# Kernel tuning notes

Hardware: AMD Instinct MI355X
Metric: run time of the kernel (lower is better)

The kernel has to match this reference:

```python
import jax, jax.numpy as jnp
import numpy as np

# --- SOM geometry constants (match init_kwargs) ---
MAP_ROWS, MAP_COLS = 32, 32
N_PROTO = MAP_ROWS * MAP_COLS
SIGMA = 1.0
PBC = True


def _build_neighborhood():
    """Gaussian neighborhood h[i,j]=exp(-dist(i,j)^2/(2*sigma^2)) on a hexagonal
    grid with periodic boundary conditions (faithful to Neighborhoods(...,'Hexagons','grid',PBC=True))."""
    rr, cc = np.meshgrid(np.arange(MAP_ROWS), np.arange(MAP_COLS), indexing='ij')
    # hexagonal lattice coordinates: odd rows shifted by 0.5, row spacing sqrt(3)/2
    x = cc + 0.5 * (rr % 2)
    y = rr * (np.sqrt(3.0) / 2.0)
    pos = np.stack([x.ravel(), y.ravel()], axis=1).astype(np.float64)  # [M, 2]
    diff = pos[:, None, :] - pos[None, :, :]                            # [M, M, 2]
    if PBC:
        width = float(MAP_COLS)
        height = MAP_ROWS * (np.sqrt(3.0) / 2.0)
        d2 = np.full((N_PROTO, N_PROTO), np.inf)
        for sx in (-1.0, 0.0, 1.0):
            for sy in (-1.0, 0.0, 1.0):
                dx = diff[..., 0] + sx * width
                dy = diff[..., 1] + sy * height
                d2 = np.minimum(d2, dx * dx + dy * dy)
    else:
        d2 = (diff ** 2).sum(-1)
    return np.exp(-d2 / (2.0 * SIGMA ** 2)).astype(np.float32)         # [M, M]


H = jnp.asarray(_build_neighborhood())  # constant [M, M] neighborhood matrix


def setup_inputs() -> dict:
    key = jax.random.key(0)
    k1, k2 = jax.random.split(key)
    inputs = jax.random.normal(k1, (16384, 256), dtype=jnp.float32)
    prototypes = jax.random.normal(k2, (N_PROTO, 256), dtype=jnp.float32) * 0.05
    return {"inputs": inputs, "prototypes": prototypes}


def reference(inputs, prototypes):
    # squared euclidean distances d[n, m] = ||x_n - p_m||^2, computed without
    # materializing the (N, M, D) broadcast intermediate
    x2 = jnp.sum(inputs * inputs, axis=1, keepdims=True)        # [N, 1]
    p2 = jnp.sum(prototypes * prototypes, axis=1)               # [M]
    d = x2 - 2.0 * (inputs @ prototypes.T) + p2[None, :]        # [N, M]
    energies = H @ d.T                                          # [M, N]
    bmus = jnp.argmin(energies, axis=0)                         # [N]
    out = 0.5 * jnp.take_along_axis(energies, bmus[None, :], axis=0)  # [1, N]
    return out
```

## Files before the change

### kernel.cpp

```cpp
#include <hip/hip_runtime.h>
#include <hip/hip_bf16.h>
#include <math.h>

#define D 256
#define NPROTO 1024
#define WR 13
#define WC 18
#define WJ (WR * WC)
#define JSUB 59
#define GMAT_BLOCKS (NPROTO / 4)
#define XPREP_BLOCKS (16384 / 8)

#define WAITVM(N) asm volatile("s_waitcnt vmcnt(" #N ")" ::: "memory")

typedef __attribute__((ext_vector_type(8))) short short8;
typedef __attribute__((ext_vector_type(4))) float f32x4;

__device__ __forceinline__ short f2bf(float f) {
    union { __hip_bfloat16 b; short s; } u;
    u.b = __float2bfloat16(f);
    return u.s;
}

__device__ __forceinline__ void gload_lds16(void* lds, const void* g) {
    __builtin_amdgcn_global_load_lds(
        (const __attribute__((address_space(1))) unsigned*)g,
        (__attribute__((address_space(3))) unsigned*)lds, 16, 0, 0);
}

__device__ __forceinline__ void proto_pos(int idx, double& x, double& y) {
    int r = idx >> 5, c = idx & 31;
    x = (double)c + 0.5 * (double)(r & 1);
    y = (double)r * 0.86602540378443864676;
}

__device__ __forceinline__ float hval(int i, int j) {
    double xi, yi, xj, yj;
    proto_pos(i, xi, yi);
    proto_pos(j, xj, yj);
    double dx0 = xi - xj, dy0 = yi - yj;
    const double W = 32.0;
    const double Hh = 27.712812921102035;
    double best = 1e300;
#pragma unroll
    for (int sx = -1; sx <= 1; ++sx) {
        double dx = dx0 + (double)sx * W;
#pragma unroll
        for (int sy = -1; sy <= 1; ++sy) {
            double dy = dy0 + (double)sy * Hh;
            double d2 = dx * dx + dy * dy;
            best = fmin(best, d2);
        }
    }
    return (float)exp(-0.5 * best);
}

__global__ void __launch_bounds__(256) prep_kernel(
    const float* __restrict__ X, const float* __restrict__ P,
    short* __restrict__ Xg, short* __restrict__ GbF,
    float* __restrict__ x2, float* __restrict__ hsum, float* __restrict__ hp2,
    unsigned* __restrict__ out) {
    int t = threadIdx.x;
    int bx = blockIdx.x;

    if (bx >= GMAT_BLOCKS) {
        int row = (bx - GMAT_BLOCKS) * 8 + (t >> 5);
        int g = t & 31;
        const float4* src = reinterpret_cast<const float4*>(X + (size_t)row * D) + g * 2;
        float4 a = src[0], b = src[1];
        float s = a.x * a.x + a.y * a.y + a.z * a.z + a.w * a.w +
                  b.x * b.x + b.y * b.y + b.z * b.z + b.w * b.w;
        s += __shfl_xor(s, 1);
        s += __shfl_xor(s, 2);
        s += __shfl_xor(s, 4);
        s += __shfl_xor(s, 8);
        s += __shfl_xor(s, 16);
        if (g == 0) x2[row] = s;
        short8 w;
        w[0] = f2bf(a.x); w[1] = f2bf(a.y); w[2] = f2bf(a.z); w[3] = f2bf(a.w);
        w[4] = f2bf(b.x); w[5] = f2bf(b.y); w[6] = f2bf(b.z); w[7] = f2bf(b.w);
        int sw = ((g * 8) & 63) ^ ((row & 7) << 3);
        *reinterpret_cast<short8*>(Xg + (size_t)row * D + ((g >> 3) << 6) + sw) = w;
        if (t < 8) out[(bx - GMAT_BLOCKS) * 8 + t] = 0x7f800000u;
        return;
    }

    __shared__ float ht[4][WJ];
    __shared__ int jrow[WJ];
    __shared__ __align__(16) float gpart[4][4][256];
    __shared__ float hqred[4][4];
    __shared__ float hsred[4][4];
    int i0 = bx * 4;
    int r0 = i0 >> 5, c0 = i0 & 31;

    for (int u = t; u < WJ; u += 256) {
        int jr = (r0 + (u / WC) - 6 + 32) & 31;
        int jc = (c0 + (u % WC) - 7 + 32) & 31;
        int j = jr * 32 + jc;
        jrow[u] = j;
#pragma unroll
        for (int s = 0; s < 4; ++s) ht[s][u] = hval(i0 + s, j);
    }
    __syncthreads();

    int w = t >> 6, lane = t & 63;
    int j0 = w * JSUB;
    int j1 = (j0 + JSUB < WJ) ? j0 + JSUB : WJ;
    f32x4 g[4] = {{0.f, 0.f, 0.f, 0.f}, {0.f, 0.f, 0.f, 0.f},
                  {0.f, 0.f, 0.f, 0.f}, {0.f, 0.f, 0.f, 0.f}};
    float hqp[4] = {0.f, 0.f, 0.f, 0.f};
    float hsp[4] = {0.f, 0.f, 0.f, 0.f};
    for (int u = j0; u < j1; ++u) {
        f32x4 pv = *reinterpret_cast<const f32x4*>(P + (size_t)jrow[u] * D + lane * 4);
        float q = pv[0] * pv[0] + pv[1] * pv[1] + pv[2] * pv[2] + pv[3] * pv[3];
#pragma unroll
        for (int s = 0; s < 4; ++s) {
            float h = ht[s][u];
            g[s][0] = fmaf(h, pv[0], g[s][0]);
            g[s][1] = fmaf(h, pv[1], g[s][1]);
            g[s][2] = fmaf(h, pv[2], g[s][2]);
            g[s][3] = fmaf(h, pv[3], g[s][3]);
            hqp[s] = fmaf(h, q, hqp[s]);
            hsp[s] += h;
        }
    }
#pragma unroll
    for (int s = 0; s < 4; ++s)
        *reinterpret_cast<f32x4*>(&gpart[w][s][lane * 4]) = g[s];
#pragma unroll
    for (int s = 0; s < 4; ++s) {
#pragma unroll
        for (int off = 1; off < 64; off <<= 1) hqp[s] += __shfl_xor(hqp[s], off);
    }
    if (lane == 0) {
#pragma unroll
        for (int s = 0; s < 4; ++s) { hqred[w][s] = hqp[s]; hsred[w][s] = hsp[s]; }
    }
    __syncthreads();

    {
        int s = t >> 6;
        f32x4 gs = *reinterpret_cast<const f32x4*>(&gpart[0][s][lane * 4]);
#pragma unroll
        for (int ww = 1; ww < 4; ++ww) {
            f32x4 gp = *reinterpret_cast<const f32x4*>(&gpart[ww][s][lane * 4]);
            gs[0] += gp[0]; gs[1] += gp[1]; gs[2] += gp[2]; gs[3] += gp[3];
        }
        float h0 = __shfl_down(gs[0], 1);
        float h1 = __shfl_down(gs[1], 1);
        float h2 = __shfl_down(gs[2], 1);
        float h3 = __shfl_down(gs[3], 1);
        if (!(lane & 1)) {
            int c = lane >> 1;
            int kg = c >> 2;
            int q = c & 3;
            int i = i0 + s;
            int Ig = i >> 4;
            short8 wv;
            wv[0] = f2bf(gs[0]); wv[1] = f2bf(gs[1]); wv[2] = f2bf(gs[2]); wv[3] = f2bf(gs[3]);
            wv[4] = f2bf(h0);    wv[5] = f2bf(h1);    wv[6] = f2bf(h2);    wv[7] = f2bf(h3);
            *reinterpret_cast<short8*>(
                GbF + ((size_t)(Ig * 8 + kg) << 9) + ((i & 15) + 16 * q) * 8) = wv;
        }
    }
    if (t < 4) {
        hsum[i0 + t] = hsred[0][t] + hsred[1][t] + hsred[2][t] + hsred[3][t];
    } else if (t < 8) {
        int s = t - 4;
        hp2[i0 + s] = hqred[0][s] + hqred[1][s] + hqred[2][s] + hqred[3][s];
    }
}

__global__ void __launch_bounds__(256) som7_kernel(
    const short* __restrict__ Xg, const short* __restrict__ GbF,
    const float* __restrict__ x2, const float* __restrict__ hsum,
    const float* __restrict__ hp2, unsigned* __restrict__ out) {
    __shared__ __align__(16) short Xs[2][128 * 64];
    __shared__ float red[2][128];

    const int t = threadIdx.x;
    const int lane = t & 63;
    const int wid = t >> 6;
    const int wr = wid >> 1;
    const int wc = wid & 1;
    const int lm = lane & 15;
    const int lq = lane >> 4;
    const int n0 = blockIdx.x * 128;
    const int ib0 = blockIdx.y * 128;
    const int Igbase = (ib0 >> 4) + wc * 4;

    f32x4 acc[4][4];
#pragma unroll
    for (int m = 0; m < 4; ++m)
#pragma unroll
        for (int n = 0; n < 4; ++n) acc[m][n] = (f32x4){0.f, 0.f, 0.f, 0.f};

    auto stage_X = [&](int xb, int kt) {
#pragma unroll
        for (int q = 0; q < 4; ++q) {
            int row = q * 32 + (t >> 3);
            gload_lds16((char*)(&Xs[xb][0]) + q * 4096 + t * 16,
                        Xg + (size_t)(n0 + row) * D + kt * 64 + (t & 7) * 8);
        }
    };

    stage_X(0, 0);

#pragma unroll
    for (int kt = 0; kt < 4; ++kt) {
        short8 b0[4], b1[4];
#pragma unroll
        for (int n = 0; n < 4; ++n) {
            const short* fb = GbF + ((size_t)((Igbase + n) * 8 + kt * 2) << 9) + lane * 8;
            b0[n] = *reinterpret_cast<const short8*>(fb);
            b1[n] = *reinterpret_cast<const short8*>(fb + 512);
        }
        __builtin_amdgcn_sched_barrier(0);
        if (kt < 3) stage_X((kt + 1) & 1, kt + 1);
        if (kt < 3) { WAITVM(12); } else { WAITVM(8); }
        __builtin_amdgcn_sched_barrier(0);
        __builtin_amdgcn_s_barrier();

        const short* xb = &Xs[kt & 1][0];
        {
            const int off = (lq * 8) ^ ((lm & 7) << 3);
            short8 a[4];
#pragma unroll
            for (int m = 0; m < 4; ++m)
                a[m] = *reinterpret_cast<const short8*>(
                    &xb[(wr * 64 + m * 16 + lm) * 64 + off]);
            if (kt < 3) { WAITVM(8); } else { WAITVM(4); }
            __builtin_amdgcn_s_setprio(1);
#pragma unroll
            for (int m = 0; m < 4; ++m)
#pragma unroll
                for (int n = 0; n < 4; ++n)
                    acc[m][n] = __builtin_amdgcn_mfma_f32_16x16x32_bf16(a[m], b0[n], acc[m][n], 0, 0, 0);
            __builtin_amdgcn_s_setprio(0);
        }
        {
            const int off = (32 + lq * 8) ^ ((lm & 7) << 3);
            short8 a[4];
#pragma unroll
            for (int m = 0; m < 4; ++m)
                a[m] = *reinterpret_cast<const short8*>(
                    &xb[(wr * 64 + m * 16 + lm) * 64 + off]);
            if (kt < 3) { WAITVM(4); } else { WAITVM(0); }
            __builtin_amdgcn_s_setprio(1);
#pragma unroll
            for (int m = 0; m < 4; ++m)
#pragma unroll
                for (int n = 0; n < 4; ++n)
                    acc[m][n] = __builtin_amdgcn_mfma_f32_16x16x32_bf16(a[m], b1[n], acc[m][n], 0, 0, 0);
            __builtin_amdgcn_s_setprio(0);
        }
    }

    float x2v[4][4];
#pragma unroll
    for (int m = 0; m < 4; ++m)
#pragma unroll
        for (int j = 0; j < 4; ++j)
            x2v[m][j] = x2[n0 + wr * 64 + m * 16 + lq * 4 + j];

    float rmin[4][4];
#pragma unroll
    for (int m = 0; m < 4; ++m)
#pragma unroll
        for (int j = 0; j < 4; ++j) rmin[m][j] = 3.4e38f;

#pragma unroll
    for (int ni = 0; ni < 4; ++ni) {
        int ig = ib0 + wc * 64 + ni * 16 + lm;
        float hs = hsum[ig];
        float hq = hp2[ig];
#pragma unroll
        for (int m = 0; m < 4; ++m)
#pragma unroll
            for (int j = 0; j < 4; ++j) {
                float e = fmaf(hs, x2v[m][j], hq) - 2.0f * acc[m][ni][j];
                rmin[m][j] = fminf(rmin[m][j], e);
            }
    }

#pragma unroll
    for (int m = 0; m < 4; ++m)
#pragma unroll
        for (int j = 0; j < 4; ++j) {
            float v = rmin[m][j];
            v = fminf(v, __shfl_xor(v, 1));
            v = fminf(v, __shfl_xor(v, 2));
            v = fminf(v, __shfl_xor(v, 4));
            v = fminf(v, __shfl_xor(v, 8));
            rmin[m][j] = v;
        }
    if (lm == 0) {
#pragma unroll
        for (int m = 0; m < 4; ++m)
#pragma unroll
            for (int j = 0; j < 4; ++j)
                red[wc][wr * 64 + m * 16 + lq * 4 + j] = rmin[m][j];
    }
    __syncthreads();
    if (t < 128) {
        float v = fminf(red[0][t], red[1][t]);
        atomicMin(out + n0 + t, __float_as_uint(0.5f * v));
    }
}

extern "C" void kernel_launch(void* const* d_in, const int* in_sizes, int n_in,
                              void* d_out, int out_size, void* d_ws, size_t ws_size,
                              hipStream_t stream) {
    const float* X = (const float*)d_in[0];
    const float* P = (const float*)d_in[1];
    unsigned* out = (unsigned*)d_out;
    int N = in_sizes[0] / D;

    float* ws = (float*)d_ws;
    float* hsum = ws + 1024;
    float* hp2 = ws + 2048;
    float* x2 = ws + 4096;
    short* GbF = (short*)(ws + 32768);
    short* Xg = (short*)(ws + 262144);

    prep_kernel<<<GMAT_BLOCKS + XPREP_BLOCKS, 256, 0, stream>>>(
        X, P, Xg, GbF, x2, hsum, hp2, out);
    som7_kernel<<<dim3(N / 128, NPROTO / 128), 256, 0, stream>>>(
        Xg, GbF, x2, hsum, hp2, out);
}
```

Baseline: 34.58 us.

## Keep input tile in registers and sweep all prototypes per block

The X preprocessing now writes inputs in MFMA fragment order through an LDS transpose, so the main kernel can load its A operands straight into registers instead of staging them via LDS. The main kernel covers all 1024 prototypes per 64-row block, with 8 waves each sweeping a quarter of the prototypes. It reduces the minimum across waves in LDS and writes the output directly. This removes the atomicMin, the output initialisation and the LDS double-buffer pipeline. The trade-off is that every block streams the whole G matrix from cache, and the grid is a single dimension of 256 blocks, which may lower parallelism and raise register pressure.

```diff
diff --git a/kernel.cpp b/kernel.cpp
--- a/kernel.cpp
+++ b/kernel.cpp
@@ -8,10 +8,8 @@
 #define WC 18
 #define WJ (WR * WC)
 #define JSUB 59
-#define GMAT_BLOCKS (NPROTO / 4)
-#define XPREP_BLOCKS (16384 / 8)
-
-#define WAITVM(N) asm volatile("s_waitcnt vmcnt(" #N ")" ::: "memory")
+#define GMAT_BLOCKS 256
+#define XPREP_BLOCKS 512
 
 typedef __attribute__((ext_vector_type(8))) short short8;
 typedef __attribute__((ext_vector_type(4))) float f32x4;
@@ -20,12 +18,6 @@
     union { __hip_bfloat16 b; short s; } u;
     u.b = __float2bfloat16(f);
     return u.s;
-}
-
-__device__ __forceinline__ void gload_lds16(void* lds, const void* g) {
-    __builtin_amdgcn_global_load_lds(
-        (const __attribute__((address_space(1))) unsigned*)g,
-        (__attribute__((address_space(3))) unsigned*)lds, 16, 0, 0);
 }
 
 __device__ __forceinline__ void proto_pos(int idx, double& x, double& y) {
@@ -55,33 +47,49 @@
     return (float)exp(-0.5 * best);
 }
 
+
 __global__ void __launch_bounds__(256) prep_kernel(
     const float* __restrict__ X, const float* __restrict__ P,
-    short* __restrict__ Xg, short* __restrict__ GbF,
-    float* __restrict__ x2, float* __restrict__ hsum, float* __restrict__ hp2,
-    unsigned* __restrict__ out) {
+    short* __restrict__ XgF, short* __restrict__ GbF,
+    float* __restrict__ x2, float* __restrict__ hsum, float* __restrict__ hp2) {
     int t = threadIdx.x;
     int bx = blockIdx.x;
 
     if (bx >= GMAT_BLOCKS) {
-        int row = (bx - GMAT_BLOCKS) * 8 + (t >> 5);
-        int g = t & 31;
-        const float4* src = reinterpret_cast<const float4*>(X + (size_t)row * D) + g * 2;
-        float4 a = src[0], b = src[1];
-        float s = a.x * a.x + a.y * a.y + a.z * a.z + a.w * a.w +
-                  b.x * b.x + b.y * b.y + b.z * b.z + b.w * b.w;
-        s += __shfl_xor(s, 1);
-        s += __shfl_xor(s, 2);
-        s += __shfl_xor(s, 4);
-        s += __shfl_xor(s, 8);
-        s += __shfl_xor(s, 16);
-        if (g == 0) x2[row] = s;
-        short8 w;
-        w[0] = f2bf(a.x); w[1] = f2bf(a.y); w[2] = f2bf(a.z); w[3] = f2bf(a.w);
-        w[4] = f2bf(b.x); w[5] = f2bf(b.y); w[6] = f2bf(b.z); w[7] = f2bf(b.w);
-        int sw = ((g * 8) & 63) ^ ((row & 7) << 3);
-        *reinterpret_cast<short8*>(Xg + (size_t)row * D + ((g >> 3) << 6) + sw) = w;
-        if (t < 8) out[(bx - GMAT_BLOCKS) * 8 + t] = 0x7f800000u;
+        __shared__ float xs[32][260];
+        int base = (bx - GMAT_BLOCKS) * 32;
+        int row = t >> 3;
+        int seg = t & 7;
+        const float4* src = reinterpret_cast<const float4*>(X + (size_t)(base + row) * D) + seg * 8;
+        float sq = 0.f;
+#pragma unroll
+        for (int p = 0; p < 8; ++p) {
+            float4 v = src[p];
+            sq += v.x * v.x + v.y * v.y + v.z * v.z + v.w * v.w;
+            *reinterpret_cast<float4*>(&xs[row][seg * 32 + p * 4]) = v;
+        }
+        sq += __shfl_xor(sq, 1);
+        sq += __shfl_xor(sq, 2);
+        sq += __shfl_xor(sq, 4);
+        if (seg == 0) x2[base + row] = sq;
+        __syncthreads();
+
+        int w = t >> 6, l = t & 63;
+        int g = w & 1;
+        int lr = g * 16 + (l & 15);
+        int q = l >> 4;
+        int Ng = (base >> 4) + g;
+#pragma unroll
+        for (int c = 0; c < 4; ++c) {
+            int kg = (w >> 1) * 4 + c;
+            const float* sp = &xs[lr][kg * 32 + q * 8];
+            float4 a = *reinterpret_cast<const float4*>(sp);
+            float4 b = *reinterpret_cast<const float4*>(sp + 4);
+            short8 wv;
+            wv[0] = f2bf(a.x); wv[1] = f2bf(a.y); wv[2] = f2bf(a.z); wv[3] = f2bf(a.w);
+            wv[4] = f2bf(b.x); wv[5] = f2bf(b.y); wv[6] = f2bf(b.z); wv[7] = f2bf(b.w);
+            *reinterpret_cast<short8*>(XgF + (((size_t)Ng * 8 + kg) << 9) + l * 8) = wv;
+        }
         return;
     }
 
@@ -160,7 +168,7 @@
             wv[0] = f2bf(gs[0]); wv[1] = f2bf(gs[1]); wv[2] = f2bf(gs[2]); wv[3] = f2bf(gs[3]);
             wv[4] = f2bf(h0);    wv[5] = f2bf(h1);    wv[6] = f2bf(h2);    wv[7] = f2bf(h3);
             *reinterpret_cast<short8*>(
-                GbF + ((size_t)(Ig * 8 + kg) << 9) + ((i & 15) + 16 * q) * 8) = wv;
+                GbF + (((size_t)Ig * 8 + kg) << 9) + ((i & 15) + 16 * q) * 8) = wv;
         }
     }
     if (t < 4) {
@@ -171,120 +179,94 @@
     }
 }
 
-__global__ void __launch_bounds__(256) som7_kernel(
-    const short* __restrict__ Xg, const short* __restrict__ GbF,
+__global__ void __launch_bounds__(512, 2) som9_kernel(
+    const short* __restrict__ XgF, const short* __restrict__ GbF,
     const float* __restrict__ x2, const float* __restrict__ hsum,
-    const float* __restrict__ hp2, unsigned* __restrict__ out) {
-    __shared__ __align__(16) short Xs[2][128 * 64];
-    __shared__ float red[2][128];
+    const float* __restrict__ hp2, float* __restrict__ out) {
+    __shared__ float red[4][64];
 
     const int t = threadIdx.x;
-    const int lane = t & 63;
+    const int l = t & 63;
     const int wid = t >> 6;
-    const int wr = wid >> 1;
-    const int wc = wid & 1;
-    const int lm = lane & 15;
-    const int lq = lane >> 4;
-    const int n0 = blockIdx.x * 128;
-    const int ib0 = blockIdx.y * 128;
-    const int Igbase = (ib0 >> 4) + wc * 4;
-
-    f32x4 acc[4][4];
-#pragma unroll
-    for (int m = 0; m < 4; ++m)
-#pragma unroll
-        for (int n = 0; n < 4; ++n) acc[m][n] = (f32x4){0.f, 0.f, 0.f, 0.f};
-
-    auto stage_X = [&](int xb, int kt) {
-#pragma unroll
-        for (int q = 0; q < 4; ++q) {
-            int row = q * 32 + (t >> 3);
-            gload_lds16((char*)(&Xs[xb][0]) + q * 4096 + t * 16,
-                        Xg + (size_t)(n0 + row) * D + kt * 64 + (t & 7) * 8);
-        }
-    };
-
-    stage_X(0, 0);
-
-#pragma unroll
-    for (int kt = 0; kt < 4; ++kt) {
-        short8 b0[4], b1[4];
-#pragma unroll
-        for (int n = 0; n < 4; ++n) {
-            const short* fb = GbF + ((size_t)((Igbase + n) * 8 + kt * 2) << 9) + lane * 8;
-            b0[n] = *reinterpret_cast<const short8*>(fb);
-            b1[n] = *reinterpret_cast<const short8*>(fb + 512);
-        }
-        __builtin_amdgcn_sched_barrier(0);
-        if (kt < 3) stage_X((kt + 1) & 1, kt + 1);
-        if (kt < 3) { WAITVM(12); } else { WAITVM(8); }
-        __builtin_amdgcn_sched_barrier(0);
-        __builtin_amdgcn_s_barrier();
-
-        const short* xb = &Xs[kt & 1][0];
-        {
-            const int off = (lq * 8) ^ ((lm & 7) << 3);
-            short8 a[4];
-#pragma unroll
-            for (int m = 0; m < 4; ++m)
-                a[m] = *reinterpret_cast<const short8*>(
-                    &xb[(wr * 64 + m * 16 + lm) * 64 + off]);
-            if (kt < 3) { WAITVM(8); } else { WAITVM(4); }
-            __builtin_amdgcn_s_setprio(1);
-#pragma unroll
-            for (int m = 0; m < 4; ++m)
-#pragma unroll
-                for (int n = 0; n < 4; ++n)
-                    acc[m][n] = __builtin_amdgcn_mfma_f32_16x16x32_bf16(a[m], b0[n], acc[m][n], 0, 0, 0);
-            __builtin_amdgcn_s_setprio(0);
-        }
-        {
-            const int off = (32 + lq * 8) ^ ((lm & 7) << 3);
-            short8 a[4];
-#pragma unroll
-            for (int m = 0; m < 4; ++m)
-                a[m] = *reinterpret_cast<const short8*>(
-                    &xb[(wr * 64 + m * 16 + lm) * 64 + off]);
-            if (kt < 3) { WAITVM(4); } else { WAITVM(0); }
-            __builtin_amdgcn_s_setprio(1);
-#pragma unroll
-            for (int m = 0; m < 4; ++m)
-#pragma unroll
-                for (int n = 0; n < 4; ++n)
-                    acc[m][n] = __builtin_amdgcn_mfma_f32_16x16x32_bf16(a[m], b1[n], acc[m][n], 0, 0, 0);
-            __builtin_amdgcn_s_setprio(0);
-        }
-    }
-
-    float x2v[4][4];
-#pragma unroll
-    for (int m = 0; m < 4; ++m)
+    const int rg = wid >> 2;
+    const int iq = wid & 3;
+    const int lm = l & 15;
+    const int lq = l >> 4;
+    const int n0 = blockIdx.x * 64;
+
+    short8 A_[4][2][2];
+    const int NgBase = (n0 >> 4) + rg * 2;
+#pragma unroll
+    for (int kt = 0; kt < 4; ++kt)
+#pragma unroll
+        for (int kk = 0; kk < 2; ++kk)
+#pragma unroll
+            for (int m = 0; m < 2; ++m)
+                A_[kt][kk][m] = *reinterpret_cast<const short8*>(
+                    XgF + (((size_t)(NgBase + m) * 8 + kt * 2 + kk) << 9) + l * 8);
+
+    float hs_[8][2], hq_[8][2];
+#pragma unroll
+    for (int ic = 0; ic < 8; ++ic)
+#pragma unroll
+        for (int n = 0; n < 2; ++n) {
+            int ig = iq * 256 + ic * 32 + n * 16 + lm;
+            hs_[ic][n] = hsum[ig];
+            hq_[ic][n] = hp2[ig];
+        }
+    float x2v[2][4];
+#pragma unroll
+    for (int m = 0; m < 2; ++m)
 #pragma unroll
         for (int j = 0; j < 4; ++j)
-            x2v[m][j] = x2[n0 + wr * 64 + m * 16 + lq * 4 + j];
-
-    float rmin[4][4];
-#pragma unroll
-    for (int m = 0; m < 4; ++m)
+            x2v[m][j] = x2[n0 + rg * 32 + m * 16 + lq * 4 + j];
+
+    float rmin[2][4];
+#pragma unroll
+    for (int m = 0; m < 2; ++m)
 #pragma unroll
         for (int j = 0; j < 4; ++j) rmin[m][j] = 3.4e38f;
 
 #pragma unroll
-    for (int ni = 0; ni < 4; ++ni) {
-        int ig = ib0 + wc * 64 + ni * 16 + lm;
-        float hs = hsum[ig];
-        float hq = hp2[ig];
-#pragma unroll
-        for (int m = 0; m < 4; ++m)
-#pragma unroll
-            for (int j = 0; j < 4; ++j) {
-                float e = fmaf(hs, x2v[m][j], hq) - 2.0f * acc[m][ni][j];
-                rmin[m][j] = fminf(rmin[m][j], e);
-            }
-    }
-
-#pragma unroll
-    for (int m = 0; m < 4; ++m)
+    for (int ic = 0; ic < 8; ++ic) {
+        f32x4 acc[2][2];
+#pragma unroll
+        for (int m = 0; m < 2; ++m)
+#pragma unroll
+            for (int n = 0; n < 2; ++n) acc[m][n] = (f32x4){0.f, 0.f, 0.f, 0.f};
+#pragma unroll
+        for (int kt = 0; kt < 4; ++kt) {
+            short8 b[2][2];
+#pragma unroll
+            for (int n = 0; n < 2; ++n)
+#pragma unroll
+                for (int kk = 0; kk < 2; ++kk)
+                    b[n][kk] = *reinterpret_cast<const short8*>(
+                        GbF + (((size_t)(iq * 16 + ic * 2 + n) * 8 + kt * 2 + kk) << 9) + l * 8);
+#pragma unroll
+            for (int m = 0; m < 2; ++m)
+#pragma unroll
+                for (int n = 0; n < 2; ++n)
+#pragma unroll
+                    for (int kk = 0; kk < 2; ++kk)
+                        acc[m][n] = __builtin_amdgcn_mfma_f32_16x16x32_bf16(
+                            A_[kt][kk][m], b[n][kk], acc[m][n], 0, 0, 0);
+        }
+#pragma unroll
+        for (int n = 0; n < 2; ++n) {
+            float hs = hs_[ic][n], hq = hq_[ic][n];
+#pragma unroll
+            for (int m = 0; m < 2; ++m)
+#pragma unroll
+                for (int j = 0; j < 4; ++j) {
+                    float e = fmaf(hs, x2v[m][j], hq) - 2.0f * acc[m][n][j];
+                    rmin[m][j] = fminf(rmin[m][j], e);
+                }
+        }
+    }
+
+#pragma unroll
+    for (int m = 0; m < 2; ++m)
 #pragma unroll
         for (int j = 0; j < 4; ++j) {
             float v = rmin[m][j];
@@ -296,15 +278,15 @@
         }
     if (lm == 0) {
 #pragma unroll
-        for (int m = 0; m < 4; ++m)
+        for (int m = 0; m < 2; ++m)
 #pragma unroll
             for (int j = 0; j < 4; ++j)
-                red[wc][wr * 64 + m * 16 + lq * 4 + j] = rmin[m][j];
+                red[iq][rg * 32 + m * 16 + lq * 4 + j] = rmin[m][j];
     }
     __syncthreads();
-    if (t < 128) {
-        float v = fminf(red[0][t], red[1][t]);
-        atomicMin(out + n0 + t, __float_as_uint(0.5f * v));
+    if (t < 64) {
+        float v = fminf(fminf(red[0][t], red[1][t]), fminf(red[2][t], red[3][t]));
+        out[n0 + t] = 0.5f * v;
     }
 }
 
@@ -313,7 +295,7 @@
                               hipStream_t stream) {
     const float* X = (const float*)d_in[0];
     const float* P = (const float*)d_in[1];
-    unsigned* out = (unsigned*)d_out;
+    float* out = (float*)d_out;
     int N = in_sizes[0] / D;
 
     float* ws = (float*)d_ws;
@@ -321,10 +303,9 @@
     float* hp2 = ws + 2048;
     float* x2 = ws + 4096;
     short* GbF = (short*)(ws + 32768);
-    short* Xg = (short*)(ws + 262144);
+    short* XgF = (short*)(ws + 262144);
 
     prep_kernel<<<GMAT_BLOCKS + XPREP_BLOCKS, 256, 0, stream>>>(
-        X, P, Xg, GbF, x2, hsum, hp2, out);
-    som7_kernel<<<dim3(N / 128, NPROTO / 128), 256, 0, stream>>>(
-        Xg, GbF, x2, hsum, hp2, out);
-}
+        X, P, XgF, GbF, x2, hsum, hp2);
+    som9_kernel<<<N / 64, 512, 0, stream>>>(XgF, GbF, x2, hsum, hp2, out);
+}
```

Measured after the change: 37.67 us. +8.9%, slower.

## Stage both GEMM operands through LDS with k-slab layout and swizzled block order

Applied to the files above, without the earlier changes.

X and the neighborhood-weighted prototype matrix G are now written by the prep kernel into k-sliced 32-column slabs with an XOR swizzle. The main kernel streams both operands into double-buffered LDS with global_load_lds over 8 k-steps, replacing direct per-wave register loads of G. It also uses a 1D grid with a remapped block order so that neighbouring blocks share tiles, sets launch_bounds occupancy to 4, and has the X-prep blocks handle 32 rows each. The aim is fewer redundant global loads of G and better cache locality, at the cost of more barriers per k-step and a hardcoded N.

```diff
diff --git a/kernel.cpp b/kernel.cpp
--- a/kernel.cpp
+++ b/kernel.cpp
@@ -4,17 +4,22 @@
 
 #define D 256
 #define NPROTO 1024
-#define WR 13
-#define WC 18
-#define WJ (WR * WC)
+#define NROWS 16384
+#define WRr 13
+#define WCc 18
+#define WJ (WRr * WCc)
 #define JSUB 59
 #define GMAT_BLOCKS (NPROTO / 4)
-#define XPREP_BLOCKS (16384 / 8)
+#define XPREP_BLOCKS (NROWS / 32)
 
 #define WAITVM(N) asm volatile("s_waitcnt vmcnt(" #N ")" ::: "memory")
 
 typedef __attribute__((ext_vector_type(8))) short short8;
 typedef __attribute__((ext_vector_type(4))) float f32x4;
+
+__device__ __forceinline__ int swz_key(int row) {
+    return (row & 3) ^ ((row >> 2) & 3);
+}
 
 __device__ __forceinline__ short f2bf(float f) {
     union { __hip_bfloat16 b; short s; } u;
@@ -55,33 +60,41 @@
     return (float)exp(-0.5 * best);
 }
 
+
 __global__ void __launch_bounds__(256) prep_kernel(
     const float* __restrict__ X, const float* __restrict__ P,
-    short* __restrict__ Xg, short* __restrict__ GbF,
+    short* __restrict__ XgS, short* __restrict__ GbS,
     float* __restrict__ x2, float* __restrict__ hsum, float* __restrict__ hp2,
     unsigned* __restrict__ out) {
     int t = threadIdx.x;
     int bx = blockIdx.x;
 
     if (bx >= GMAT_BLOCKS) {
-        int row = (bx - GMAT_BLOCKS) * 8 + (t >> 5);
+        int base0 = (bx - GMAT_BLOCKS) * 32;
         int g = t & 31;
-        const float4* src = reinterpret_cast<const float4*>(X + (size_t)row * D) + g * 2;
-        float4 a = src[0], b = src[1];
-        float s = a.x * a.x + a.y * a.y + a.z * a.z + a.w * a.w +
-                  b.x * b.x + b.y * b.y + b.z * b.z + b.w * b.w;
-        s += __shfl_xor(s, 1);
-        s += __shfl_xor(s, 2);
-        s += __shfl_xor(s, 4);
-        s += __shfl_xor(s, 8);
-        s += __shfl_xor(s, 16);
-        if (g == 0) x2[row] = s;
-        short8 w;
-        w[0] = f2bf(a.x); w[1] = f2bf(a.y); w[2] = f2bf(a.z); w[3] = f2bf(a.w);
-        w[4] = f2bf(b.x); w[5] = f2bf(b.y); w[6] = f2bf(b.z); w[7] = f2bf(b.w);
-        int sw = ((g * 8) & 63) ^ ((row & 7) << 3);
-        *reinterpret_cast<short8*>(Xg + (size_t)row * D + ((g >> 3) << 6) + sw) = w;
-        if (t < 8) out[(bx - GMAT_BLOCKS) * 8 + t] = 0x7f800000u;
+        int kt = g >> 2;
+        int slot = g & 3;
+#pragma unroll
+        for (int it = 0; it < 4; ++it) {
+            int row = base0 + it * 8 + (t >> 5);
+            const float4* src = reinterpret_cast<const float4*>(X + (size_t)row * D) + g * 2;
+            float4 a = src[0], b = src[1];
+            float s = a.x * a.x + a.y * a.y + a.z * a.z + a.w * a.w +
+                      b.x * b.x + b.y * b.y + b.z * b.z + b.w * b.w;
+            s += __shfl_xor(s, 1);
+            s += __shfl_xor(s, 2);
+            s += __shfl_xor(s, 4);
+            s += __shfl_xor(s, 8);
+            s += __shfl_xor(s, 16);
+            if (g == 0) x2[row] = s;
+            short8 w;
+            w[0] = f2bf(a.x); w[1] = f2bf(a.y); w[2] = f2bf(a.z); w[3] = f2bf(a.w);
+            w[4] = f2bf(b.x); w[5] = f2bf(b.y); w[6] = f2bf(b.z); w[7] = f2bf(b.w);
+            *reinterpret_cast<short8*>(
+                XgS + (size_t)kt * (NROWS * 32) + (size_t)row * 32 +
+                ((slot ^ swz_key(row)) << 3)) = w;
+        }
+        if (t < 32) out[base0 + t] = 0x7f800000u;
         return;
     }
 
@@ -94,8 +107,8 @@
     int r0 = i0 >> 5, c0 = i0 & 31;
 
     for (int u = t; u < WJ; u += 256) {
-        int jr = (r0 + (u / WC) - 6 + 32) & 31;
-        int jc = (c0 + (u % WC) - 7 + 32) & 31;
+        int jr = (r0 + (u / WCc) - 6 + 32) & 31;
+        int jc = (c0 + (u % WCc) - 7 + 32) & 31;
         int j = jr * 32 + jc;
         jrow[u] = j;
 #pragma unroll
@@ -152,15 +165,15 @@
         float h3 = __shfl_down(gs[3], 1);
         if (!(lane & 1)) {
             int c = lane >> 1;
-            int kg = c >> 2;
-            int q = c & 3;
+            int kt = c >> 2;
+            int slot = c & 3;
             int i = i0 + s;
-            int Ig = i >> 4;
             short8 wv;
             wv[0] = f2bf(gs[0]); wv[1] = f2bf(gs[1]); wv[2] = f2bf(gs[2]); wv[3] = f2bf(gs[3]);
             wv[4] = f2bf(h0);    wv[5] = f2bf(h1);    wv[6] = f2bf(h2);    wv[7] = f2bf(h3);
             *reinterpret_cast<short8*>(
-                GbF + ((size_t)(Ig * 8 + kg) << 9) + ((i & 15) + 16 * q) * 8) = wv;
+                GbS + (size_t)kt * (NPROTO * 32) + (size_t)i * 32 +
+                ((slot ^ swz_key(i)) << 3)) = wv;
         }
     }
     if (t < 4) {
@@ -171,11 +184,12 @@
     }
 }
 
-__global__ void __launch_bounds__(256) som7_kernel(
-    const short* __restrict__ Xg, const short* __restrict__ GbF,
+__global__ void __launch_bounds__(256, 4) som8_kernel(
+    const short* __restrict__ XgS, const short* __restrict__ GbS,
     const float* __restrict__ x2, const float* __restrict__ hsum,
     const float* __restrict__ hp2, unsigned* __restrict__ out) {
-    __shared__ __align__(16) short Xs[2][128 * 64];
+    __shared__ __align__(16) short Xs[2][128 * 32];
+    __shared__ __align__(16) short Gs[2][128 * 32];
     __shared__ float red[2][128];
 
     const int t = threadIdx.x;
@@ -185,9 +199,12 @@
     const int wc = wid & 1;
     const int lm = lane & 15;
     const int lq = lane >> 4;
-    const int n0 = blockIdx.x * 128;
-    const int ib0 = blockIdx.y * 128;
-    const int Igbase = (ib0 >> 4) + wc * 4;
+    const int key = (lm & 3) ^ ((lm >> 2) & 3);
+
+    const int lin = blockIdx.x;
+    const int w1024 = ((lin & 7) << 7) | (lin >> 3);
+    const int n0 = (w1024 >> 3) * 128;
+    const int ib0 = (w1024 & 7) * 128;
 
     f32x4 acc[4][4];
 #pragma unroll
@@ -195,65 +212,46 @@
 #pragma unroll
         for (int n = 0; n < 4; ++n) acc[m][n] = (f32x4){0.f, 0.f, 0.f, 0.f};
 
-    auto stage_X = [&](int xb, int kt) {
-#pragma unroll
-        for (int q = 0; q < 4; ++q) {
-            int row = q * 32 + (t >> 3);
-            gload_lds16((char*)(&Xs[xb][0]) + q * 4096 + t * 16,
-                        Xg + (size_t)(n0 + row) * D + kt * 64 + (t & 7) * 8);
-        }
+    auto stage = [&](int b, int kt) {
+#pragma unroll
+        for (int q = 0; q < 2; ++q)
+            gload_lds16((char*)(&Xs[b][0]) + q * 4096 + t * 16,
+                        XgS + (size_t)kt * (NROWS * 32) +
+                        (size_t)(n0 + q * 64 + (t >> 2)) * 32 + ((t & 3) << 3));
+#pragma unroll
+        for (int q = 0; q < 2; ++q)
+            gload_lds16((char*)(&Gs[b][0]) + q * 4096 + t * 16,
+                        GbS + (size_t)kt * (NPROTO * 32) +
+                        (size_t)(ib0 + q * 64 + (t >> 2)) * 32 + ((t & 3) << 3));
     };
 
-    stage_X(0, 0);
-
-#pragma unroll
-    for (int kt = 0; kt < 4; ++kt) {
-        short8 b0[4], b1[4];
-#pragma unroll
-        for (int n = 0; n < 4; ++n) {
-            const short* fb = GbF + ((size_t)((Igbase + n) * 8 + kt * 2) << 9) + lane * 8;
-            b0[n] = *reinterpret_cast<const short8*>(fb);
-            b1[n] = *reinterpret_cast<const short8*>(fb + 512);
-        }
-        __builtin_amdgcn_sched_barrier(0);
-        if (kt < 3) stage_X((kt + 1) & 1, kt + 1);
-        if (kt < 3) { WAITVM(12); } else { WAITVM(8); }
+    stage(0, 0);
+
+#pragma unroll
+    for (int p = 0; p < 8; ++p) {
+        if (p < 7) stage((p + 1) & 1, p + 1);
+        if (p < 7) { WAITVM(4); } else { WAITVM(0); }
         __builtin_amdgcn_sched_barrier(0);
         __builtin_amdgcn_s_barrier();
 
-        const short* xb = &Xs[kt & 1][0];
-        {
-            const int off = (lq * 8) ^ ((lm & 7) << 3);
-            short8 a[4];
-#pragma unroll
-            for (int m = 0; m < 4; ++m)
-                a[m] = *reinterpret_cast<const short8*>(
-                    &xb[(wr * 64 + m * 16 + lm) * 64 + off]);
-            if (kt < 3) { WAITVM(8); } else { WAITVM(4); }
-            __builtin_amdgcn_s_setprio(1);
-#pragma unroll
-            for (int m = 0; m < 4; ++m)
-#pragma unroll
-                for (int n = 0; n < 4; ++n)
-                    acc[m][n] = __builtin_amdgcn_mfma_f32_16x16x32_bf16(a[m], b0[n], acc[m][n], 0, 0, 0);
-            __builtin_amdgcn_s_setprio(0);
-        }
-        {
-            const int off = (32 + lq * 8) ^ ((lm & 7) << 3);
-            short8 a[4];
-#pragma unroll
-            for (int m = 0; m < 4; ++m)
-                a[m] = *reinterpret_cast<const short8*>(
-                    &xb[(wr * 64 + m * 16 + lm) * 64 + off]);
-            if (kt < 3) { WAITVM(4); } else { WAITVM(0); }
-            __builtin_amdgcn_s_setprio(1);
-#pragma unroll
-            for (int m = 0; m < 4; ++m)
-#pragma unroll
-                for (int n = 0; n < 4; ++n)
-                    acc[m][n] = __builtin_amdgcn_mfma_f32_16x16x32_bf16(a[m], b1[n], acc[m][n], 0, 0, 0);
-            __builtin_amdgcn_s_setprio(0);
-        }
+        const short* xb = &Xs[p & 1][0];
+        const short* gb = &Gs[p & 1][0];
+        const int so = (lq ^ key) << 3;
+        short8 a[4], b[4];
+#pragma unroll
+        for (int m = 0; m < 4; ++m)
+            a[m] = *reinterpret_cast<const short8*>(&xb[(wr * 64 + m * 16 + lm) * 32 + so]);
+#pragma unroll
+        for (int n = 0; n < 4; ++n)
+            b[n] = *reinterpret_cast<const short8*>(&gb[(wc * 64 + n * 16 + lm) * 32 + so]);
+        __builtin_amdgcn_s_setprio(1);
+#pragma unroll
+        for (int m = 0; m < 4; ++m)
+#pragma unroll
+            for (int n = 0; n < 4; ++n)
+                acc[m][n] = __builtin_amdgcn_mfma_f32_16x16x32_bf16(a[m], b[n], acc[m][n], 0, 0, 0);
+        __builtin_amdgcn_s_setprio(0);
+        __builtin_amdgcn_s_barrier();
     }
 
     float x2v[4][4];
@@ -314,17 +312,16 @@
     const float* X = (const float*)d_in[0];
     const float* P = (const float*)d_in[1];
     unsigned* out = (unsigned*)d_out;
-    int N = in_sizes[0] / D;
+    (void)in_sizes; (void)n_in; (void)out_size; (void)ws_size;
 
     float* ws = (float*)d_ws;
     float* hsum = ws + 1024;
     float* hp2 = ws + 2048;
     float* x2 = ws + 4096;
-    short* GbF = (short*)(ws + 32768);
-    short* Xg = (short*)(ws + 262144);
+    short* GbS = (short*)(ws + 32768);
+    short* XgS = (short*)(ws + 262144);
 
     prep_kernel<<<GMAT_BLOCKS + XPREP_BLOCKS, 256, 0, stream>>>(
-        X, P, Xg, GbF, x2, hsum, hp2, out);
-    som7_kernel<<<dim3(N / 128, NPROTO / 128), 256, 0, stream>>>(
-        Xg, GbF, x2, hsum, hp2, out);
-}
+        X, P, XgS, GbS, x2, hsum, hp2, out);
+    som8_kernel<<<1024, 256, 0, stream>>>(XgS, GbS, x2, hsum, hp2, out);
+}
```

Result: faster. 32.37 us (-6.4%).
